# Kernel tuning notes

Measured on AMD Instinct MI355X. Metric: run time of the kernel, lower is better.

## Reference

```python
import jax, jax.numpy as jnp
import numpy as np
from jax import lax

B, S, V, E, H = 64, 512, 50000, 300, 256


def _run_lstm(x, w_ih, w_hh, b_ih, b_hh, reverse):
    # x: [B,S,D]; w_ih: [4H,D]; w_hh: [4H,H]. PyTorch gate order: i,f,g,o.
    gx = jnp.einsum('bsd,gd->sbg', x, w_ih) + b_ih + b_hh  # [S,B,4H]
    Hh = w_hh.shape[1]

    def step(carry, g):
        h, c = carry
        g = g + h @ w_hh.T
        i, f, gg, o = jnp.split(g, 4, axis=-1)
        c = jax.nn.sigmoid(f) * c + jax.nn.sigmoid(i) * jnp.tanh(gg)
        h = jax.nn.sigmoid(o) * jnp.tanh(c)
        return (h, c), h

    init = (jnp.zeros((x.shape[0], Hh), x.dtype), jnp.zeros((x.shape[0], Hh), x.dtype))
    _, hs = lax.scan(step, init, gx, reverse=reverse)  # outputs aligned to input time order
    return jnp.swapaxes(hs, 0, 1)  # [B,S,H]


def _bilstm(x, wif, whf, bif, bhf, wib, whb, bib, bhb):
    fwd = _run_lstm(x, wif, whf, bif, bhf, False)
    bwd = _run_lstm(x, wib, whb, bib, bhb, True)
    return jnp.concatenate([fwd, bwd], axis=-1)  # [B,S,2H]


def setup_inputs() -> dict:
    key = jax.random.key(0)
    ks = iter(jax.random.split(key, 32))
    k = 1.0 / np.sqrt(H)
    u = lambda shape: jax.random.uniform(next(ks), shape, jnp.float32, -k, k)
    inp = {
        'input_ids': jax.random.randint(next(ks), (B, S), 0, V),
        'labels': jax.random.uniform(next(ks), (B, S), jnp.float32),
        'input_masks': jnp.ones((B, S), jnp.int64),
        'emb': jax.random.normal(next(ks), (V, E), jnp.float32) * 0.1,
    }
    # layer 0 (input E), layer 1 (input 2H); forward and backward directions
    for layer, d_in in ((0, E), (1, 2 * H)):
        for direc in ('f', 'b'):
            inp[f'w_ih_l{layer}{direc}'] = u((4 * H, d_in))
            inp[f'w_hh_l{layer}{direc}'] = u((4 * H, H))
            inp[f'b_ih_l{layer}{direc}'] = u((4 * H,))
            inp[f'b_hh_l{layer}{direc}'] = u((4 * H,))
    inp['w_lin'] = u((H,))
    inp['b_lin'] = u(())
    return inp


def reference(input_ids, labels, input_masks, emb,
              w_ih_l0f, w_hh_l0f, b_ih_l0f, b_hh_l0f,
              w_ih_l0b, w_hh_l0b, b_ih_l0b, b_hh_l0b,
              w_ih_l1f, w_hh_l1f, b_ih_l1f, b_hh_l1f,
              w_ih_l1b, w_hh_l1b, b_ih_l1b, b_hh_l1b,
              w_lin, b_lin):
    x = emb[input_ids]  # one-shot gather, replaces the double python loop: [B,S,E]
    h1 = _bilstm(x, w_ih_l0f, w_hh_l0f, b_ih_l0f, b_hh_l0f,
                 w_ih_l0b, w_hh_l0b, b_ih_l0b, b_hh_l0b)
    h2 = _bilstm(h1, w_ih_l1f, w_hh_l1f, b_ih_l1f, b_hh_l1f,
                 w_ih_l1b, w_hh_l1b, b_ih_l1b, b_hh_l1b)  # [B,S,2H]
    b, s = h2.shape[0], h2.shape[1]
    mean_dir = h2.reshape(b, s, 2, H).mean(axis=2)  # mean over directions
    scores = jax.nn.sigmoid(jnp.einsum('bsh,h->bs', mean_dir, w_lin) + b_lin)
    mask = input_masks.astype(scores.dtype)
    err = (scores - labels) ** 2 * mask
    loss = jnp.mean(jnp.sum(err, axis=1) / jnp.sum(mask, axis=1))
    return scores, loss
```

## Files before the change

kernel.cpp:

```cpp
#include <hip/hip_runtime.h>
#include <hip/hip_bf16.h>
#include <stdint.h>

#define B_  64
#define S_  512
#define E_  300
#define H_  256
#define T_  (B_*S_)
#define G4H 1024

using half8  = __attribute__((ext_vector_type(8))) _Float16;
using half4  = __attribute__((ext_vector_type(4))) _Float16;
using float4v = __attribute__((ext_vector_type(4))) float;

union H2 { _Float16 h[2]; uint32_t u; };

__device__ inline float sigm(float x) { return 1.f / (1.f + __expf(-x)); }
__device__ inline float tanhf_(float x) {
  float cx = fminf(fmaxf(x, -15.f), 15.f);
  float e = __expf(2.f * cx);
  return (e - 1.f) / (e + 1.f);
}

__global__ __launch_bounds__(256) void k_prep_wih(const float* __restrict__ wf,
    const float* __restrict__ wb, _Float16* __restrict__ Bt,
    int KIN, int KP, int total)
{
  int idx = blockIdx.x * 256 + threadIdx.x;
  if (idx >= total) return;
  int n = idx / KP, k = idx % KP;
  int dd = n >> 10, nn = n & 1023;
  int row = (nn & 3) * 256 + (nn >> 2);
  const float* src = dd ? wb : wf;
  Bt[idx] = (_Float16)(k < KIN ? src[row * KIN + k] : 0.f);
}

__global__ __launch_bounds__(256) void k_prep_whh(const float* __restrict__ wf,
    const float* __restrict__ wb, _Float16* __restrict__ Wr)
{
  int idx = blockIdx.x * 256 + threadIdx.x;
  int dd = idx >> 18;
  int rem = idx & 262143;
  int n = rem >> 8, k = rem & 255;
  int row = (n & 3) * 256 + (n >> 2);
  Wr[idx] = (_Float16)((dd ? wb : wf)[row * 256 + k]);
}

__global__ void k_prep_bias(const float* __restrict__ bif, const float* __restrict__ bhf,
    const float* __restrict__ bib, const float* __restrict__ bhb, float* __restrict__ bias)
{
  int n = blockIdx.x * 256 + threadIdx.x;
  int dd = n >> 10, nn = n & 1023;
  int row = (nn & 3) * 256 + (nn >> 2);
  bias[n] = dd ? (bib[row] + bhb[row]) : (bif[row] + bhf[row]);
}

__global__ __launch_bounds__(256) void k_gather(const int* __restrict__ ids,
    const float* __restrict__ emb, _Float16* __restrict__ xbf)
{
  int idx = blockIdx.x * 256 + threadIdx.x;
  int tt = idx / 40;
  int ch = idx % 40;
  int b = tt & 63, s = tt >> 6;
  int id = ids[b * S_ + s];
  const float* src = emb + (size_t)id * E_ + ch * 8;
  half8 v;
#pragma unroll
  for (int e = 0; e < 8; ++e) {
    int k = ch * 8 + e;
    v[e] = (_Float16)(k < E_ ? src[e] : 0.f);
  }
  *(half8*)(xbf + (size_t)tt * 320 + ch * 8) = v;
}

template<int K>
__global__ __launch_bounds__(256) void k_gemm(const _Float16* __restrict__ A,
    const _Float16* __restrict__ Bt, const float* __restrict__ bias,
    _Float16* __restrict__ gx)
{
  __shared__ _Float16 sA[128 * 72];
  __shared__ _Float16 sB[128 * 72];
  const int tid = threadIdx.x;
  const int t0 = blockIdx.y * 128;
  const int n0 = blockIdx.x * 128;
  const int lane = tid & 63, wid = tid >> 6;
  const int l15 = lane & 15, q = lane >> 4;
  const int wm = wid & 1, wn = wid >> 1;

  float4v acc[4][4] = {};

  for (int kt = 0; kt < K / 64; ++kt) {
    __syncthreads();
#pragma unroll
    for (int c = 0; c < 4; ++c) {
      int f = tid * 4 + c;
      int row = f >> 3, seg = f & 7;
      *(half8*)&sA[row * 72 + seg * 8] =
          *(const half8*)(A + (size_t)(t0 + row) * K + kt * 64 + seg * 8);
      *(half8*)&sB[row * 72 + seg * 8] =
          *(const half8*)(Bt + (size_t)(n0 + row) * K + kt * 64 + seg * 8);
    }
    __syncthreads();
#pragma unroll
    for (int kk = 0; kk < 2; ++kk) {
      half8 a[4], b[4];
#pragma unroll
      for (int mt = 0; mt < 4; ++mt)
        a[mt] = *(const half8*)&sA[(wm * 64 + mt * 16 + l15) * 72 + kk * 32 + q * 8];
#pragma unroll
      for (int nt = 0; nt < 4; ++nt)
        b[nt] = *(const half8*)&sB[(wn * 64 + nt * 16 + l15) * 72 + kk * 32 + q * 8];
#pragma unroll
      for (int mt = 0; mt < 4; ++mt)
#pragma unroll
        for (int nt = 0; nt < 4; ++nt)
          acc[mt][nt] = __builtin_amdgcn_mfma_f32_16x16x32_f16(a[mt], b[nt], acc[mt][nt], 0, 0, 0);
    }
  }

#pragma unroll
  for (int mt = 0; mt < 4; ++mt) {
#pragma unroll
    for (int nt = 0; nt < 4; ++nt) {
      int token = t0 + wm * 64 + mt * 16 + q * 4;
      int n = n0 + wn * 64 + nt * 16 + l15;
      float bs = bias[n];
      size_t base = (size_t)(n >> 10) * ((size_t)T_ * G4H) + (size_t)token * G4H + (n & 1023);
#pragma unroll
      for (int r = 0; r < 4; ++r)
        gx[base + (size_t)r * G4H] = (_Float16)(acc[mt][nt][r] + bs);
    }
  }
}

template<int LAYER>
__global__ __launch_bounds__(256, 1) void k_rec(const _Float16* __restrict__ gx,
    const _Float16* __restrict__ Wr, uint64_t* __restrict__ hx,
    _Float16* __restrict__ h1bf, float* __restrict__ pd2,
    const float* __restrict__ w_lin)
{
  const int bx = blockIdx.x;
  const int d = bx >> 4, rg = (bx >> 2) & 3, g = bx & 3;
  const int tid = threadIdx.x;
  const int lane = tid & 63, wv = tid >> 6;
  const int l15 = lane & 15, q = lane >> 4;
  const int b0g = g * 16;
  const int n0g = rg * 256;

  __shared__ _Float16 hstage[16 * 288];
  __shared__ float    preS[16 * 260];

  for (int i = tid; i < 16 * 288 / 2; i += 256)
    ((uint32_t*)hstage)[i] = 0u;

  half8 wfrag[4][8];
#pragma unroll
  for (int nt = 0; nt < 4; ++nt)
#pragma unroll
    for (int kt = 0; kt < 8; ++kt)
      wfrag[nt][kt] = *(const half8*)(Wr +
          (size_t)(d * G4H + n0g + wv * 64 + nt * 16 + l15) * H_ + kt * 32 + q * 8);

  const int bl = tid >> 4;
  const int jl4 = (tid & 15) * 4;
  const int bglob = b0g + bl;
  const int jg = rg * 64 + jl4;
  float wl[4];
#pragma unroll
  for (int cc = 0; cc < 4; ++cc) wl[cc] = w_lin[jg + cc];
  float creg[4] = {0.f, 0.f, 0.f, 0.f};

  uint64_t* gbase = hx + (size_t)(d * 4 + g) * 2 * 2048;

  int pidx[6];
  {
    int c6 = 0;
#pragma unroll
    for (int qq = 1; qq <= 3; ++qq) {
      int q2 = (rg + qq) & 3;
      pidx[c6++] = q2 * 512 + tid * 2;
      pidx[c6++] = q2 * 512 + tid * 2 + 1;
    }
  }

  for (int t = 0; t < S_; ++t) {
    const int time = d ? (S_ - 1 - t) : t;

    const _Float16* gxp = gx + ((size_t)d * T_ + (size_t)time * B_ + bglob) * G4H
                             + n0g + (tid & 15) * 16;
    half8 gxa = *(const half8*)(gxp);
    half8 gxb = *(const half8*)(gxp + 8);

    if (t > 0) {
      const uint64_t* slot = gbase + (size_t)(t & 1) * 2048;
      uint64_t got[6];
      unsigned pend = 0x3f;
      while (pend) {
#pragma unroll
        for (int w = 0; w < 6; ++w) {
          if (pend & (1u << w)) {
            uint64_t v = __hip_atomic_load(slot + pidx[w], __ATOMIC_RELAXED,
                                           __HIP_MEMORY_SCOPE_AGENT);
            if ((uint32_t)(v >> 32) == (uint32_t)t) { got[w] = v; pend &= ~(1u << w); }
          }
        }
      }
#pragma unroll
      for (int w = 0; w < 6; ++w) {
        int gw = pidx[w];
        int q2 = gw >> 9, loc = gw & 511;
        int sb = loc >> 5, jp = loc & 31;
        ((uint32_t*)hstage)[sb * 144 + q2 * 32 + jp] = (uint32_t)got[w];
      }
    }
    __syncthreads();

    float4v acc[4] = {};
#pragma unroll
    for (int kt = 0; kt < 8; ++kt) {
      half8 a = *(const half8*)&hstage[l15 * 288 + kt * 32 + q * 8];
#pragma unroll
      for (int nt = 0; nt < 4; ++nt)
        acc[nt] = __builtin_amdgcn_mfma_f32_16x16x32_f16(a, wfrag[nt][kt], acc[nt], 0, 0, 0);
    }

#pragma unroll
    for (int nt = 0; nt < 4; ++nt)
#pragma unroll
      for (int r = 0; r < 4; ++r)
        preS[(q * 4 + r) * 260 + wv * 64 + nt * 16 + l15] = acc[nt][r];
    __syncthreads();

    half4 hv4;
    float partial = 0.f;
#pragma unroll
    for (int cc = 0; cc < 4; ++cc) {
      float4v p = *(const float4v*)&preS[bl * 260 + (jl4 + cc) * 4];
      float gxi = (float)(cc < 2 ? gxa[cc * 4 + 0] : gxb[(cc - 2) * 4 + 0]);
      float gxf = (float)(cc < 2 ? gxa[cc * 4 + 1] : gxb[(cc - 2) * 4 + 1]);
      float gxg = (float)(cc < 2 ? gxa[cc * 4 + 2] : gxb[(cc - 2) * 4 + 2]);
      float gxo = (float)(cc < 2 ? gxa[cc * 4 + 3] : gxb[(cc - 2) * 4 + 3]);
      float gi = p[0] + gxi, gf = p[1] + gxf, gg = p[2] + gxg, go = p[3] + gxo;
      float cv = sigm(gf) * creg[cc] + sigm(gi) * tanhf_(gg);
      float hv = sigm(go) * tanhf_(cv);
      creg[cc] = cv;
      hv4[cc] = (_Float16)hv;
      if (LAYER == 1) partial += 0.5f * hv * wl[cc];
    }

    *(half4*)&hstage[bl * 288 + jg] = hv4;

    {
      H2 p0; p0.h[0] = hv4[0]; p0.h[1] = hv4[1];
      H2 p1; p1.h[0] = hv4[2]; p1.h[1] = hv4[3];
      uint64_t tg = ((uint64_t)(uint32_t)(t + 1)) << 32;
      uint64_t* slot = gbase + (size_t)((t + 1) & 1) * 2048;
      int wb = rg * 512 + bl * 32 + (jl4 >> 1);
      __hip_atomic_store(slot + wb,     tg | p0.u, __ATOMIC_RELAXED, __HIP_MEMORY_SCOPE_AGENT);
      __hip_atomic_store(slot + wb + 1, tg | p1.u, __ATOMIC_RELAXED, __HIP_MEMORY_SCOPE_AGENT);
    }

    if (LAYER == 0) {
      *(half4*)(h1bf + ((size_t)time * B_ + bglob) * 512 + d * H_ + jg) = hv4;
    } else {
      partial += __shfl_xor(partial, 1);
      partial += __shfl_xor(partial, 2);
      partial += __shfl_xor(partial, 4);
      partial += __shfl_xor(partial, 8);
      if ((tid & 15) == 0)
        atomicAdd(pd2 + ((size_t)d * B_ + bglob) * S_ + time, partial);
    }
  }
}

__global__ __launch_bounds__(256) void k_final(const float* __restrict__ pd2,
    const float* __restrict__ labels, const int* __restrict__ masks,
    const float* __restrict__ b_lin, float* __restrict__ out)
{
  int b = blockIdx.x;
  int tid = threadIdx.x;
  float bl = b_lin[0];
  float se = 0.f, sm = 0.f;
  for (int s = tid; s < S_; s += 256) {
    float p = pd2[(size_t)b * S_ + s] + pd2[(size_t)(B_ + b) * S_ + s];
    float sc = sigm(p + bl);
    out[b * S_ + s] = sc;
    float m = (float)masks[b * S_ + s];
    float e = sc - labels[b * S_ + s];
    se += e * e * m;
    sm += m;
  }
  for (int off = 1; off < 64; off <<= 1) {
    se += __shfl_xor(se, off);
    sm += __shfl_xor(sm, off);
  }
  __shared__ float rs[4], rm[4];
  int wid = tid >> 6;
  if ((tid & 63) == 0) { rs[wid] = se; rm[wid] = sm; }
  __syncthreads();
  if (tid == 0) {
    float te = 0.f, tm = 0.f;
    for (int w = 0; w < 4; ++w) { te += rs[w]; tm += rm[w]; }
    atomicAdd(out + T_, (te / tm) * (1.f / 64.f));
  }
}

extern "C" void kernel_launch(void* const* d_in, const int* in_sizes, int n_in,
                              void* d_out, int out_size, void* d_ws, size_t ws_size,
                              hipStream_t stream)
{
  (void)in_sizes; (void)n_in; (void)out_size; (void)ws_size;
  const int*   ids    = (const int*)d_in[0];
  const float* labels = (const float*)d_in[1];
  const int*   masks  = (const int*)d_in[2];
  const float* emb    = (const float*)d_in[3];
  const float* w_ih_0f = (const float*)d_in[4];
  const float* w_hh_0f = (const float*)d_in[5];
  const float* b_ih_0f = (const float*)d_in[6];
  const float* b_hh_0f = (const float*)d_in[7];
  const float* w_ih_0b = (const float*)d_in[8];
  const float* w_hh_0b = (const float*)d_in[9];
  const float* b_ih_0b = (const float*)d_in[10];
  const float* b_hh_0b = (const float*)d_in[11];
  const float* w_ih_1f = (const float*)d_in[12];
  const float* w_hh_1f = (const float*)d_in[13];
  const float* b_ih_1f = (const float*)d_in[14];
  const float* b_hh_1f = (const float*)d_in[15];
  const float* w_ih_1b = (const float*)d_in[16];
  const float* w_hh_1b = (const float*)d_in[17];
  const float* b_ih_1b = (const float*)d_in[18];
  const float* b_hh_1b = (const float*)d_in[19];
  const float* w_lin   = (const float*)d_in[20];
  const float* b_lin   = (const float*)d_in[21];
  float* out = (float*)d_out;

  char* ws = (char*)d_ws;
  size_t off = 0;
  auto alloc = [&](size_t bytes) -> char* {
    char* p = ws + off;
    off += (bytes + 255) & ~(size_t)255;
    return p;
  };
  _Float16* xbf   = (_Float16*)alloc((size_t)T_ * 320 * 2);
  _Float16* h1bf  = (_Float16*)alloc((size_t)T_ * 512 * 2);
  _Float16* gx    = (_Float16*)alloc((size_t)2 * T_ * G4H * 2);
  _Float16* Bt0   = (_Float16*)alloc((size_t)2048 * 320 * 2);
  _Float16* Bt1   = (_Float16*)alloc((size_t)2048 * 512 * 2);
  _Float16* Wr0   = (_Float16*)alloc((size_t)2 * G4H * H_ * 2);
  _Float16* Wr1   = (_Float16*)alloc((size_t)2 * G4H * H_ * 2);
  float*    bias0 = (float*)alloc(2048 * 4);
  float*    bias1 = (float*)alloc(2048 * 4);
  uint64_t* hx0   = (uint64_t*)alloc((size_t)8 * 2 * 2048 * 8);
  uint64_t* hx1   = (uint64_t*)alloc((size_t)8 * 2 * 2048 * 8);
  float*    pd2   = (float*)alloc((size_t)2 * B_ * S_ * 4);

  k_prep_wih<<<(2048 * 320) / 256, 256, 0, stream>>>(w_ih_0f, w_ih_0b, Bt0, 300, 320, 2048 * 320);
  k_prep_wih<<<(2048 * 512) / 256, 256, 0, stream>>>(w_ih_1f, w_ih_1b, Bt1, 512, 512, 2048 * 512);
  k_prep_whh<<<524288 / 256, 256, 0, stream>>>(w_hh_0f, w_hh_0b, Wr0);
  k_prep_whh<<<524288 / 256, 256, 0, stream>>>(w_hh_1f, w_hh_1b, Wr1);
  k_prep_bias<<<8, 256, 0, stream>>>(b_ih_0f, b_hh_0f, b_ih_0b, b_hh_0b, bias0);
  k_prep_bias<<<8, 256, 0, stream>>>(b_ih_1f, b_hh_1f, b_ih_1b, b_hh_1b, bias1);
  k_gather<<<(T_ * 40) / 256, 256, 0, stream>>>(ids, emb, xbf);

  hipMemsetAsync(hx0, 0, (size_t)8 * 2 * 2048 * 8, stream);
  hipMemsetAsync(hx1, 0, (size_t)8 * 2 * 2048 * 8, stream);
  hipMemsetAsync(pd2, 0, (size_t)2 * B_ * S_ * 4, stream);
  hipMemsetAsync((char*)d_out + (size_t)T_ * 4, 0, 4, stream);

  k_gemm<320><<<dim3(16, 256), 256, 0, stream>>>(xbf, Bt0, bias0, gx);
  k_rec<0><<<32, 256, 0, stream>>>(gx, Wr0, hx0, h1bf, pd2, w_lin);

  k_gemm<512><<<dim3(16, 256), 256, 0, stream>>>(h1bf, Bt1, bias1, gx);
  k_rec<1><<<32, 256, 0, stream>>>(gx, Wr1, hx1, h1bf, pd2, w_lin);

  k_final<<<64, 256, 0, stream>>>(pd2, labels, masks, b_lin, out);
}
```

Before: 3.360 ms.

## Repartition recurrent kernel into 8 gate-slices per direction cycling batch groups

The recurrent LSTM kernel now uses 16 blocks instead of 32. Each block owns a 128-wide gate slice (32 hidden units) across all 64 batch rows, processed as four 16-row batch groups in turn. The cross-block hidden-state exchange now covers all 8 slices of a direction. Polling loads and gx loads for the next batch group are prefetched while the current group's activations are computed, and __syncthreads is replaced with a raw lgkmcnt-wait barrier. The aim is to overlap the wait on one batch group with work on another and to halve per-block weight registers, at the cost of fewer CUs and serial processing of the four groups inside each block.

Result: slower. 9.280 ms (+176.2%).

```diff
diff --git a/kernel.cpp b/kernel.cpp
--- a/kernel.cpp
+++ b/kernel.cpp
@@ -21,6 +21,8 @@
   float e = __expf(2.f * cx);
   return (e - 1.f) / (e + 1.f);
 }
+
+#define BARRIER() asm volatile("s_waitcnt lgkmcnt(0)\n\ts_barrier" ::: "memory")
 
 __global__ __launch_bounds__(256) void k_prep_wih(const float* __restrict__ wf,
     const float* __restrict__ wb, _Float16* __restrict__ Bt,
@@ -140,135 +142,133 @@
     const float* __restrict__ w_lin)
 {
   const int bx = blockIdx.x;
-  const int d = bx >> 4, rg = (bx >> 2) & 3, g = bx & 3;
+  const int d = bx >> 3, rg = bx & 7;
   const int tid = threadIdx.x;
   const int lane = tid & 63, wv = tid >> 6;
   const int l15 = lane & 15, q = lane >> 4;
-  const int b0g = g * 16;
-  const int n0g = rg * 256;
-
-  __shared__ _Float16 hstage[16 * 288];
-  __shared__ float    preS[16 * 260];
-
-  for (int i = tid; i < 16 * 288 / 2; i += 256)
-    ((uint32_t*)hstage)[i] = 0u;
-
-  half8 wfrag[4][8];
-#pragma unroll
-  for (int nt = 0; nt < 4; ++nt)
+  const int n0g = rg * 128;
+
+  __shared__ _Float16 hstage[16 * 264];
+  __shared__ float    preS[16 * 136];
+
+  half8 wfrag[2][8];
+#pragma unroll
+  for (int nt = 0; nt < 2; ++nt)
 #pragma unroll
     for (int kt = 0; kt < 8; ++kt)
       wfrag[nt][kt] = *(const half8*)(Wr +
-          (size_t)(d * G4H + n0g + wv * 64 + nt * 16 + l15) * H_ + kt * 32 + q * 8);
+          (size_t)(d * G4H + n0g + wv * 32 + nt * 16 + l15) * H_ + kt * 32 + q * 8);
 
   const int bl = tid >> 4;
-  const int jl4 = (tid & 15) * 4;
-  const int bglob = b0g + bl;
-  const int jg = rg * 64 + jl4;
-  float wl[4];
-#pragma unroll
-  for (int cc = 0; cc < 4; ++cc) wl[cc] = w_lin[jg + cc];
-  float creg[4] = {0.f, 0.f, 0.f, 0.f};
-
-  uint64_t* gbase = hx + (size_t)(d * 4 + g) * 2 * 2048;
-
-  int pidx[6];
+  const int jl2 = (tid & 15) * 2;
+  const int jg = rg * 32 + jl2;
+  float wl0 = w_lin[jg], wl1 = w_lin[jg + 1];
+  float creg[4][2] = {};
+
+  uint64_t* gpool = hx + (size_t)d * 4 * 2 * 2048;
+
+  const int wpub = bl * 128 + rg * 16 + (tid & 15);
+  const int wpoll = tid * 8;
+  const int pb = wpoll >> 7;
+  const int pj = wpoll & 127;
+
+  uint64_t pv[8];
+  half8 gxv;
+
   {
-    int c6 = 0;
-#pragma unroll
-    for (int qq = 1; qq <= 3; ++qq) {
-      int q2 = (rg + qq) & 3;
-      pidx[c6++] = q2 * 512 + tid * 2;
-      pidx[c6++] = q2 * 512 + tid * 2 + 1;
-    }
+    const uint64_t* slot = gpool + 0;
+#pragma unroll
+    for (int w = 0; w < 8; ++w)
+      pv[w] = __hip_atomic_load(slot + wpoll + w, __ATOMIC_RELAXED, __HIP_MEMORY_SCOPE_AGENT);
+    const int time0 = d ? (S_ - 1) : 0;
+    gxv = *(const half8*)(gx + ((size_t)d * T_ + (size_t)time0 * B_ + bl) * G4H
+                          + n0g + jl2 * 4);
   }
 
   for (int t = 0; t < S_; ++t) {
     const int time = d ? (S_ - 1 - t) : t;
-
-    const _Float16* gxp = gx + ((size_t)d * T_ + (size_t)time * B_ + bglob) * G4H
-                             + n0g + (tid & 15) * 16;
-    half8 gxa = *(const half8*)(gxp);
-    half8 gxb = *(const half8*)(gxp + 8);
-
-    if (t > 0) {
-      const uint64_t* slot = gbase + (size_t)(t & 1) * 2048;
-      uint64_t got[6];
-      unsigned pend = 0x3f;
-      while (pend) {
-#pragma unroll
-        for (int w = 0; w < 6; ++w) {
-          if (pend & (1u << w)) {
-            uint64_t v = __hip_atomic_load(slot + pidx[w], __ATOMIC_RELAXED,
-                                           __HIP_MEMORY_SCOPE_AGENT);
-            if ((uint32_t)(v >> 32) == (uint32_t)t) { got[w] = v; pend &= ~(1u << w); }
+#pragma unroll 1
+    for (int u = 0; u < 4; ++u) {
+      {
+        const uint64_t* slot = gpool + ((size_t)u * 2 + (t & 1)) * 2048;
+        unsigned pend = 0xffu;
+        while (pend) {
+#pragma unroll
+          for (int w = 0; w < 8; ++w) {
+            if (pend & (1u << w)) {
+              if ((uint32_t)(pv[w] >> 32) == (uint32_t)t) pend &= ~(1u << w);
+              else pv[w] = __hip_atomic_load(slot + wpoll + w, __ATOMIC_RELAXED,
+                                             __HIP_MEMORY_SCOPE_AGENT);
+            }
           }
         }
       }
 #pragma unroll
-      for (int w = 0; w < 6; ++w) {
-        int gw = pidx[w];
-        int q2 = gw >> 9, loc = gw & 511;
-        int sb = loc >> 5, jp = loc & 31;
-        ((uint32_t*)hstage)[sb * 144 + q2 * 32 + jp] = (uint32_t)got[w];
-      }
-    }
-    __syncthreads();
-
-    float4v acc[4] = {};
-#pragma unroll
-    for (int kt = 0; kt < 8; ++kt) {
-      half8 a = *(const half8*)&hstage[l15 * 288 + kt * 32 + q * 8];
-#pragma unroll
-      for (int nt = 0; nt < 4; ++nt)
-        acc[nt] = __builtin_amdgcn_mfma_f32_16x16x32_f16(a, wfrag[nt][kt], acc[nt], 0, 0, 0);
-    }
-
-#pragma unroll
-    for (int nt = 0; nt < 4; ++nt)
-#pragma unroll
-      for (int r = 0; r < 4; ++r)
-        preS[(q * 4 + r) * 260 + wv * 64 + nt * 16 + l15] = acc[nt][r];
-    __syncthreads();
-
-    half4 hv4;
-    float partial = 0.f;
-#pragma unroll
-    for (int cc = 0; cc < 4; ++cc) {
-      float4v p = *(const float4v*)&preS[bl * 260 + (jl4 + cc) * 4];
-      float gxi = (float)(cc < 2 ? gxa[cc * 4 + 0] : gxb[(cc - 2) * 4 + 0]);
-      float gxf = (float)(cc < 2 ? gxa[cc * 4 + 1] : gxb[(cc - 2) * 4 + 1]);
-      float gxg = (float)(cc < 2 ? gxa[cc * 4 + 2] : gxb[(cc - 2) * 4 + 2]);
-      float gxo = (float)(cc < 2 ? gxa[cc * 4 + 3] : gxb[(cc - 2) * 4 + 3]);
-      float gi = p[0] + gxi, gf = p[1] + gxf, gg = p[2] + gxg, go = p[3] + gxo;
-      float cv = sigm(gf) * creg[cc] + sigm(gi) * tanhf_(gg);
-      float hv = sigm(go) * tanhf_(cv);
-      creg[cc] = cv;
-      hv4[cc] = (_Float16)hv;
-      if (LAYER == 1) partial += 0.5f * hv * wl[cc];
-    }
-
-    *(half4*)&hstage[bl * 288 + jg] = hv4;
-
-    {
-      H2 p0; p0.h[0] = hv4[0]; p0.h[1] = hv4[1];
-      H2 p1; p1.h[0] = hv4[2]; p1.h[1] = hv4[3];
-      uint64_t tg = ((uint64_t)(uint32_t)(t + 1)) << 32;
-      uint64_t* slot = gbase + (size_t)((t + 1) & 1) * 2048;
-      int wb = rg * 512 + bl * 32 + (jl4 >> 1);
-      __hip_atomic_store(slot + wb,     tg | p0.u, __ATOMIC_RELAXED, __HIP_MEMORY_SCOPE_AGENT);
-      __hip_atomic_store(slot + wb + 1, tg | p1.u, __ATOMIC_RELAXED, __HIP_MEMORY_SCOPE_AGENT);
-    }
-
-    if (LAYER == 0) {
-      *(half4*)(h1bf + ((size_t)time * B_ + bglob) * 512 + d * H_ + jg) = hv4;
-    } else {
-      partial += __shfl_xor(partial, 1);
-      partial += __shfl_xor(partial, 2);
-      partial += __shfl_xor(partial, 4);
-      partial += __shfl_xor(partial, 8);
-      if ((tid & 15) == 0)
-        atomicAdd(pd2 + ((size_t)d * B_ + bglob) * S_ + time, partial);
+      for (int w = 0; w < 8; ++w)
+        ((uint32_t*)hstage)[pb * 132 + pj + w] = (uint32_t)pv[w];
+      BARRIER();
+
+      float4v acc[2] = {};
+#pragma unroll
+      for (int kt = 0; kt < 8; ++kt) {
+        half8 a = *(const half8*)&hstage[l15 * 264 + kt * 32 + q * 8];
+        acc[0] = __builtin_amdgcn_mfma_f32_16x16x32_f16(a, wfrag[0][kt], acc[0], 0, 0, 0);
+        acc[1] = __builtin_amdgcn_mfma_f32_16x16x32_f16(a, wfrag[1][kt], acc[1], 0, 0, 0);
+      }
+#pragma unroll
+      for (int nt = 0; nt < 2; ++nt)
+#pragma unroll
+        for (int r = 0; r < 4; ++r)
+          preS[(q * 4 + r) * 136 + wv * 32 + nt * 16 + l15] = acc[nt][r];
+      BARRIER();
+
+      int nu = (u + 1) & 3;
+      int tn = (u == 3) ? t + 1 : t;
+      int tc = tn < S_ ? tn : S_ - 1;
+      {
+        const uint64_t* slotn = gpool + ((size_t)nu * 2 + (tc & 1)) * 2048;
+#pragma unroll
+        for (int w = 0; w < 8; ++w)
+          pv[w] = __hip_atomic_load(slotn + wpoll + w, __ATOMIC_RELAXED,
+                                    __HIP_MEMORY_SCOPE_AGENT);
+      }
+      const int timen = d ? (S_ - 1 - tc) : tc;
+      half8 gxn = *(const half8*)(gx + ((size_t)d * T_ + (size_t)timen * B_ + (nu * 16 + bl)) * G4H
+                                  + n0g + jl2 * 4);
+
+      const int bglob = u * 16 + bl;
+      float4v p0 = *(const float4v*)&preS[bl * 136 + jl2 * 4];
+      float4v p1 = *(const float4v*)&preS[bl * 136 + jl2 * 4 + 4];
+      float gi0 = p0[0] + (float)gxv[0], gf0 = p0[1] + (float)gxv[1];
+      float gg0 = p0[2] + (float)gxv[2], go0 = p0[3] + (float)gxv[3];
+      float gi1 = p1[0] + (float)gxv[4], gf1 = p1[1] + (float)gxv[5];
+      float gg1 = p1[2] + (float)gxv[6], go1 = p1[3] + (float)gxv[7];
+      float cv0 = sigm(gf0) * creg[u][0] + sigm(gi0) * tanhf_(gg0);
+      float cv1 = sigm(gf1) * creg[u][1] + sigm(gi1) * tanhf_(gg1);
+      float hv0 = sigm(go0) * tanhf_(cv0);
+      float hv1 = sigm(go1) * tanhf_(cv1);
+      creg[u][0] = cv0; creg[u][1] = cv1;
+
+      {
+        H2 hp; hp.h[0] = (_Float16)hv0; hp.h[1] = (_Float16)hv1;
+        uint64_t word = (((uint64_t)(uint32_t)(t + 1)) << 32) | hp.u;
+        uint64_t* slotw = gpool + ((size_t)u * 2 + ((t + 1) & 1)) * 2048;
+        __hip_atomic_store(slotw + wpub, word, __ATOMIC_RELAXED, __HIP_MEMORY_SCOPE_AGENT);
+      }
+
+      if (LAYER == 0) {
+        H2 hp; hp.h[0] = (_Float16)hv0; hp.h[1] = (_Float16)hv1;
+        *(uint32_t*)(h1bf + ((size_t)time * B_ + bglob) * 512 + d * H_ + jg) = hp.u;
+      } else {
+        float partial = 0.5f * (hv0 * wl0 + hv1 * wl1);
+        partial += __shfl_xor(partial, 1);
+        partial += __shfl_xor(partial, 2);
+        partial += __shfl_xor(partial, 4);
+        partial += __shfl_xor(partial, 8);
+        if ((tid & 15) == 0)
+          atomicAdd(pd2 + ((size_t)d * B_ + bglob) * S_ + time, partial);
+      }
+      gxv = gxn;
     }
   }
 }
@@ -350,8 +350,8 @@
   _Float16* Wr1   = (_Float16*)alloc((size_t)2 * G4H * H_ * 2);
   float*    bias0 = (float*)alloc(2048 * 4);
   float*    bias1 = (float*)alloc(2048 * 4);
-  uint64_t* hx0   = (uint64_t*)alloc((size_t)8 * 2 * 2048 * 8);
-  uint64_t* hx1   = (uint64_t*)alloc((size_t)8 * 2 * 2048 * 8);
+  uint64_t* hx0   = (uint64_t*)alloc((size_t)2 * 4 * 2 * 2048 * 8);
+  uint64_t* hx1   = (uint64_t*)alloc((size_t)2 * 4 * 2 * 2048 * 8);
   float*    pd2   = (float*)alloc((size_t)2 * B_ * S_ * 4);
 
   k_prep_wih<<<(2048 * 320) / 256, 256, 0, stream>>>(w_ih_0f, w_ih_0b, Bt0, 300, 320, 2048 * 320);
@@ -362,16 +362,16 @@
   k_prep_bias<<<8, 256, 0, stream>>>(b_ih_1f, b_hh_1f, b_ih_1b, b_hh_1b, bias1);
   k_gather<<<(T_ * 40) / 256, 256, 0, stream>>>(ids, emb, xbf);
 
-  hipMemsetAsync(hx0, 0, (size_t)8 * 2 * 2048 * 8, stream);
-  hipMemsetAsync(hx1, 0, (size_t)8 * 2 * 2048 * 8, stream);
+  hipMemsetAsync(hx0, 0, (size_t)2 * 4 * 2 * 2048 * 8, stream);
+  hipMemsetAsync(hx1, 0, (size_t)2 * 4 * 2 * 2048 * 8, stream);
   hipMemsetAsync(pd2, 0, (size_t)2 * B_ * S_ * 4, stream);
   hipMemsetAsync((char*)d_out + (size_t)T_ * 4, 0, 4, stream);
 
   k_gemm<320><<<dim3(16, 256), 256, 0, stream>>>(xbf, Bt0, bias0, gx);
-  k_rec<0><<<32, 256, 0, stream>>>(gx, Wr0, hx0, h1bf, pd2, w_lin);
+  k_rec<0><<<16, 256, 0, stream>>>(gx, Wr0, hx0, h1bf, pd2, w_lin);
 
   k_gemm<512><<<dim3(16, 256), 256, 0, stream>>>(h1bf, Bt1, bias1, gx);
-  k_rec<1><<<32, 256, 0, stream>>>(gx, Wr1, hx1, h1bf, pd2, w_lin);
+  k_rec<1><<<16, 256, 0, stream>>>(gx, Wr1, hx1, h1bf, pd2, w_lin);
 
   k_final<<<64, 256, 0, stream>>>(pd2, labels, masks, b_lin, out);
 }
```

## Use vectorized sc0 polling with atomic fallback for inter-block hidden-state exchange

Applied to the files above, without the earlier changes.

The recurrent kernel's cross-block hidden-state exchange now writes each tagged value twice: once with a non-coherent sc0 store into a fast buffer and once with an agent-scope atomic store into a slow buffer. Consumers poll the fast buffer with three vectorized dwordx4 loads and check the atomic buffer only every fourth round, so spin-wait latency per timestep should drop. Block-index mapping is reordered so the blocks sharing a batch group have adjacent IDs, and __syncthreads is replaced by a raw lgkmcnt wait plus s_barrier. The cost is double the store traffic and reliance on cache behaviour for the sc0 path, with the atomic path kept as a correctness fallback.

New measurement: 3.315 ms. Within noise of the previous version (-1.3%).

```diff
diff --git a/kernel.cpp b/kernel.cpp
--- a/kernel.cpp
+++ b/kernel.cpp
@@ -20,6 +20,22 @@
   float cx = fminf(fmaxf(x, -15.f), 15.f);
   float e = __expf(2.f * cx);
   return (e - 1.f) / (e + 1.f);
+}
+
+#define BARRIER() asm volatile("s_waitcnt lgkmcnt(0)\n\ts_barrier" ::: "memory")
+
+__device__ inline void ld3_sc0(const uint64_t* p0, const uint64_t* p1,
+                               const uint64_t* p2, uint4& a, uint4& b, uint4& c) {
+  asm volatile(
+      "global_load_dwordx4 %0, %3, off sc0\n\t"
+      "global_load_dwordx4 %1, %4, off sc0\n\t"
+      "global_load_dwordx4 %2, %5, off sc0\n\t"
+      "s_waitcnt vmcnt(0)"
+      : "=&v"(a), "=&v"(b), "=&v"(c)
+      : "v"(p0), "v"(p1), "v"(p2) : "memory");
+}
+__device__ inline void st_sc0(uint64_t* p, uint64_t v) {
+  asm volatile("global_store_dwordx2 %0, %1, off sc0" :: "v"(p), "v"(v) : "memory");
 }
 
 __global__ __launch_bounds__(256) void k_prep_wih(const float* __restrict__ wf,
@@ -135,12 +151,13 @@
 
 template<int LAYER>
 __global__ __launch_bounds__(256, 1) void k_rec(const _Float16* __restrict__ gx,
-    const _Float16* __restrict__ Wr, uint64_t* __restrict__ hx,
-    _Float16* __restrict__ h1bf, float* __restrict__ pd2,
-    const float* __restrict__ w_lin)
+    const _Float16* __restrict__ Wr, uint64_t* __restrict__ hxf,
+    uint64_t* __restrict__ hxs, _Float16* __restrict__ h1bf,
+    float* __restrict__ pd2, const float* __restrict__ w_lin)
 {
   const int bx = blockIdx.x;
-  const int d = bx >> 4, rg = (bx >> 2) & 3, g = bx & 3;
+  const int cg = bx & 7, rg = bx >> 3;
+  const int d = cg >> 2, g = cg & 3;
   const int tid = threadIdx.x;
   const int lane = tid & 63, wv = tid >> 6;
   const int l15 = lane & 15, q = lane >> 4;
@@ -150,16 +167,18 @@
   __shared__ _Float16 hstage[16 * 288];
   __shared__ float    preS[16 * 260];
 
-  for (int i = tid; i < 16 * 288 / 2; i += 256)
+  for (int i = tid; i < 16 * 144; i += 256)
     ((uint32_t*)hstage)[i] = 0u;
 
   half8 wfrag[4][8];
 #pragma unroll
   for (int nt = 0; nt < 4; ++nt)
 #pragma unroll
-    for (int kt = 0; kt < 8; ++kt)
+    for (int kt = 0; kt < 8; ++kt) {
       wfrag[nt][kt] = *(const half8*)(Wr +
           (size_t)(d * G4H + n0g + wv * 64 + nt * 16 + l15) * H_ + kt * 32 + q * 8);
+      asm volatile("" : "+v"(wfrag[nt][kt]));
+    }
 
   const int bl = tid >> 4;
   const int jl4 = (tid & 15) * 4;
@@ -170,18 +189,10 @@
   for (int cc = 0; cc < 4; ++cc) wl[cc] = w_lin[jg + cc];
   float creg[4] = {0.f, 0.f, 0.f, 0.f};
 
-  uint64_t* gbase = hx + (size_t)(d * 4 + g) * 2 * 2048;
-
-  int pidx[6];
-  {
-    int c6 = 0;
-#pragma unroll
-    for (int qq = 1; qq <= 3; ++qq) {
-      int q2 = (rg + qq) & 3;
-      pidx[c6++] = q2 * 512 + tid * 2;
-      pidx[c6++] = q2 * 512 + tid * 2 + 1;
-    }
-  }
+  uint64_t* fbase = hxf + (size_t)cg * 2 * 2048;
+  uint64_t* sbase = hxs + (size_t)cg * 2 * 2048;
+  const int off2 = tid * 2;
+  const int q2a = (rg + 1) & 3, q2b = (rg + 2) & 3, q2c = (rg + 3) & 3;
 
   for (int t = 0; t < S_; ++t) {
     const int time = d ? (S_ - 1 - t) : t;
@@ -192,28 +203,46 @@
     half8 gxb = *(const half8*)(gxp + 8);
 
     if (t > 0) {
-      const uint64_t* slot = gbase + (size_t)(t & 1) * 2048;
-      uint64_t got[6];
-      unsigned pend = 0x3f;
+      const uint64_t* fs = fbase + (size_t)(t & 1) * 2048;
+      const uint64_t* ss = sbase + (size_t)(t & 1) * 2048;
+      const uint32_t tt = (uint32_t)t;
+      uint32_t dat[6];
+      unsigned pend = 0x3fu;
+      int round = 0;
       while (pend) {
-#pragma unroll
-        for (int w = 0; w < 6; ++w) {
-          if (pend & (1u << w)) {
-            uint64_t v = __hip_atomic_load(slot + pidx[w], __ATOMIC_RELAXED,
-                                           __HIP_MEMORY_SCOPE_AGENT);
-            if ((uint32_t)(v >> 32) == (uint32_t)t) { got[w] = v; pend &= ~(1u << w); }
-          }
+        uint4 A, Bv, C;
+        ld3_sc0(fs + q2a * 512 + off2, fs + q2b * 512 + off2,
+                fs + q2c * 512 + off2, A, Bv, C);
+        if ((pend & 1u)  && A.y  == tt) { dat[0] = A.x;  pend &= ~1u; }
+        if ((pend & 2u)  && A.w  == tt) { dat[1] = A.z;  pend &= ~2u; }
+        if ((pend & 4u)  && Bv.y == tt) { dat[2] = Bv.x; pend &= ~4u; }
+        if ((pend & 8u)  && Bv.w == tt) { dat[3] = Bv.z; pend &= ~8u; }
+        if ((pend & 16u) && C.y  == tt) { dat[4] = C.x;  pend &= ~16u; }
+        if ((pend & 32u) && C.w  == tt) { dat[5] = C.z;  pend &= ~32u; }
+        if (pend && ((++round & 3) == 0)) {
+          const int wq[3] = {q2a, q2b, q2c};
+#pragma unroll
+          for (int k3 = 0; k3 < 3; ++k3)
+#pragma unroll
+            for (int j = 0; j < 2; ++j) {
+              int w = k3 * 2 + j;
+              if (pend & (1u << w)) {
+                uint64_t v = __hip_atomic_load(ss + wq[k3] * 512 + off2 + j,
+                                               __ATOMIC_RELAXED, __HIP_MEMORY_SCOPE_AGENT);
+                if ((uint32_t)(v >> 32) == tt) { dat[w] = (uint32_t)v; pend &= ~(1u << w); }
+              }
+            }
         }
       }
-#pragma unroll
-      for (int w = 0; w < 6; ++w) {
-        int gw = pidx[w];
-        int q2 = gw >> 9, loc = gw & 511;
-        int sb = loc >> 5, jp = loc & 31;
-        ((uint32_t*)hstage)[sb * 144 + q2 * 32 + jp] = (uint32_t)got[w];
-      }
-    }
-    __syncthreads();
+      const int sb = tid >> 4, jp = (tid & 15) * 2;
+      uint2 va; va.x = dat[0]; va.y = dat[1];
+      uint2 vb; vb.x = dat[2]; vb.y = dat[3];
+      uint2 vc; vc.x = dat[4]; vc.y = dat[5];
+      *(uint2*)&((uint32_t*)hstage)[sb * 144 + q2a * 32 + jp] = va;
+      *(uint2*)&((uint32_t*)hstage)[sb * 144 + q2b * 32 + jp] = vb;
+      *(uint2*)&((uint32_t*)hstage)[sb * 144 + q2c * 32 + jp] = vc;
+    }
+    BARRIER();
 
     float4v acc[4] = {};
 #pragma unroll
@@ -223,13 +252,12 @@
       for (int nt = 0; nt < 4; ++nt)
         acc[nt] = __builtin_amdgcn_mfma_f32_16x16x32_f16(a, wfrag[nt][kt], acc[nt], 0, 0, 0);
     }
-
 #pragma unroll
     for (int nt = 0; nt < 4; ++nt)
 #pragma unroll
       for (int r = 0; r < 4; ++r)
         preS[(q * 4 + r) * 260 + wv * 64 + nt * 16 + l15] = acc[nt][r];
-    __syncthreads();
+    BARRIER();
 
     half4 hv4;
     float partial = 0.f;
@@ -248,17 +276,21 @@
       if (LAYER == 1) partial += 0.5f * hv * wl[cc];
     }
 
-    *(half4*)&hstage[bl * 288 + jg] = hv4;
-
     {
       H2 p0; p0.h[0] = hv4[0]; p0.h[1] = hv4[1];
       H2 p1; p1.h[0] = hv4[2]; p1.h[1] = hv4[3];
-      uint64_t tg = ((uint64_t)(uint32_t)(t + 1)) << 32;
-      uint64_t* slot = gbase + (size_t)((t + 1) & 1) * 2048;
-      int wb = rg * 512 + bl * 32 + (jl4 >> 1);
-      __hip_atomic_store(slot + wb,     tg | p0.u, __ATOMIC_RELAXED, __HIP_MEMORY_SCOPE_AGENT);
-      __hip_atomic_store(slot + wb + 1, tg | p1.u, __ATOMIC_RELAXED, __HIP_MEMORY_SCOPE_AGENT);
-    }
+      uint32_t tg = (uint32_t)(t + 1);
+      uint64_t w0 = ((uint64_t)tg << 32) | p0.u;
+      uint64_t w1 = ((uint64_t)tg << 32) | p1.u;
+      uint64_t* fd = fbase + (size_t)((t + 1) & 1) * 2048 + rg * 512 + off2;
+      st_sc0(fd + 0, w0);
+      st_sc0(fd + 1, w1);
+      uint64_t* sd = sbase + (size_t)((t + 1) & 1) * 2048 + rg * 512 + off2;
+      __hip_atomic_store(sd + 0, w0, __ATOMIC_RELAXED, __HIP_MEMORY_SCOPE_AGENT);
+      __hip_atomic_store(sd + 1, w1, __ATOMIC_RELAXED, __HIP_MEMORY_SCOPE_AGENT);
+    }
+
+    *(half4*)&hstage[bl * 288 + jg] = hv4;
 
     if (LAYER == 0) {
       *(half4*)(h1bf + ((size_t)time * B_ + bglob) * 512 + d * H_ + jg) = hv4;
@@ -350,8 +382,10 @@
   _Float16* Wr1   = (_Float16*)alloc((size_t)2 * G4H * H_ * 2);
   float*    bias0 = (float*)alloc(2048 * 4);
   float*    bias1 = (float*)alloc(2048 * 4);
-  uint64_t* hx0   = (uint64_t*)alloc((size_t)8 * 2 * 2048 * 8);
-  uint64_t* hx1   = (uint64_t*)alloc((size_t)8 * 2 * 2048 * 8);
+  uint64_t* hxf0  = (uint64_t*)alloc((size_t)8 * 2 * 2048 * 8);
+  uint64_t* hxs0  = (uint64_t*)alloc((size_t)8 * 2 * 2048 * 8);
+  uint64_t* hxf1  = (uint64_t*)alloc((size_t)8 * 2 * 2048 * 8);
+  uint64_t* hxs1  = (uint64_t*)alloc((size_t)8 * 2 * 2048 * 8);
   float*    pd2   = (float*)alloc((size_t)2 * B_ * S_ * 4);
 
   k_prep_wih<<<(2048 * 320) / 256, 256, 0, stream>>>(w_ih_0f, w_ih_0b, Bt0, 300, 320, 2048 * 320);
@@ -362,16 +396,18 @@
   k_prep_bias<<<8, 256, 0, stream>>>(b_ih_1f, b_hh_1f, b_ih_1b, b_hh_1b, bias1);
   k_gather<<<(T_ * 40) / 256, 256, 0, stream>>>(ids, emb, xbf);
 
-  hipMemsetAsync(hx0, 0, (size_t)8 * 2 * 2048 * 8, stream);
-  hipMemsetAsync(hx1, 0, (size_t)8 * 2 * 2048 * 8, stream);
+  hipMemsetAsync(hxf0, 0, (size_t)8 * 2 * 2048 * 8, stream);
+  hipMemsetAsync(hxs0, 0, (size_t)8 * 2 * 2048 * 8, stream);
+  hipMemsetAsync(hxf1, 0, (size_t)8 * 2 * 2048 * 8, stream);
+  hipMemsetAsync(hxs1, 0, (size_t)8 * 2 * 2048 * 8, stream);
   hipMemsetAsync(pd2, 0, (size_t)2 * B_ * S_ * 4, stream);
   hipMemsetAsync((char*)d_out + (size_t)T_ * 4, 0, 4, stream);
 
   k_gemm<320><<<dim3(16, 256), 256, 0, stream>>>(xbf, Bt0, bias0, gx);
-  k_rec<0><<<32, 256, 0, stream>>>(gx, Wr0, hx0, h1bf, pd2, w_lin);
+  k_rec<0><<<32, 256, 0, stream>>>(gx, Wr0, hxf0, hxs0, h1bf, pd2, w_lin);
 
   k_gemm<512><<<dim3(16, 256), 256, 0, stream>>>(h1bf, Bt1, bias1, gx);
-  k_rec<1><<<32, 256, 0, stream>>>(gx, Wr1, hx1, h1bf, pd2, w_lin);
+  k_rec<1><<<32, 256, 0, stream>>>(gx, Wr1, hxf1, hxs1, h1bf, pd2, w_lin);
 
   k_final<<<64, 256, 0, stream>>>(pd2, labels, masks, b_lin, out);
 }
```
